# Optimization experiments

Measured on AMD Instinct MI355X. Metric: run time of the kernel, lower is better.

## Reference

```python
import jax, jax.numpy as jnp
import numpy as np

WINSIZE = 11
SIGMA = 1.5
L_RANGE = 1.0

def _gaussian_window(winsize, channel, dtype=jnp.float32):
    x = jnp.arange(winsize, dtype=dtype)
    g = jnp.exp(-((x - winsize // 2) ** 2) / (2.0 * SIGMA ** 2))
    g = g / g.sum()
    w2d = jnp.outer(g, g)                      # [ws, ws]
    # depthwise kernel [channel, 1, ws, ws] (OIHW, feature_group_count=channel)
    return jnp.broadcast_to(w2d, (channel, 1, winsize, winsize))

def _dwconv(x, w, channel):
    pad = WINSIZE // 2
    return jax.lax.conv_general_dilated(
        x, w, window_strides=(1, 1), padding=[(pad, pad), (pad, pad)],
        dimension_numbers=('NCHW', 'OIHW', 'NCHW'),
        feature_group_count=channel)

def _ssim(X, Y):
    channel = X.shape[1]
    w = _gaussian_window(WINSIZE, channel, X.dtype)
    mu1 = _dwconv(X, w, channel)
    mu2 = _dwconv(Y, w, channel)
    mu1_sq = mu1 * mu1
    mu2_sq = mu2 * mu2
    mu1_mu2 = mu1 * mu2
    sigma1_sq = _dwconv(X * X, w, channel) - mu1_sq
    sigma2_sq = _dwconv(Y * Y, w, channel) - mu2_sq
    sigma12 = _dwconv(X * Y, w, channel) - mu1_mu2
    C1 = (0.01 * L_RANGE) ** 2
    C2 = (0.03 * L_RANGE) ** 2
    ssim_map = ((2.0 * mu1_mu2 + C1) * (2.0 * sigma12 + C2)) / \
               ((mu1_sq + mu2_sq + C1) * (sigma1_sq + sigma2_sq + C2))
    return jnp.mean(ssim_map)  # sizeavg=True

def setup_inputs() -> dict:
    key = jax.random.key(0)
    k1, k2 = jax.random.split(key)
    shape = (16, 3, 512, 512)
    X = jax.random.uniform(k1, shape, dtype=jnp.float32)
    Y = jax.random.uniform(k2, shape, dtype=jnp.float32)
    return {"X": X, "Y": Y}

def reference(X, Y):
    return 1.0 - _ssim(X, Y)
```

## Files before the change

kernel.cpp:

```cpp
#include <hip/hip_runtime.h>


#define ROWS 32
#define COLS 256
#define NI   (ROWS + 10)
#define LW   (COLS + 10)
#define NIMG 48
#define NBLOCKS (NIMG * 2 * 16)
#define NPIXEL 12582912.0

__global__ __launch_bounds__(256) void ssim_row_kernel(
    const float* __restrict__ X, const float* __restrict__ Y,
    float* __restrict__ partial)
{
    __shared__ float sb[2][2][LW + 6];

    const int tid = threadIdx.x;
    const int bid = blockIdx.x;
    const int img = bid >> 5;
    const int rem = bid & 31;
    const int c0  = (rem & 1) * COLS;
    const int r0  = (rem >> 1) * ROWS;

    const float* __restrict__ Xi = X + (size_t)img * (512 * 512);
    const float* __restrict__ Yi = Y + (size_t)img * (512 * 512);

    float g[11];
    {
        float s = 0.f;
        #pragma unroll
        for (int i = 0; i < 11; ++i) {
            float d = (float)(i - 5);
            float e = expf(-d * d * (1.0f / 4.5f));
            g[i] = e; s += e;
        }
        float inv = 1.0f / s;
        #pragma unroll
        for (int i = 0; i < 11; ++i) g[i] *= inv;
    }

    const bool tail = (tid < LW - COLS);
    const int  gc0  = c0 - 5 + tid;
    const int  gc1  = gc0 + COLS;

    {
        int gr = r0 - 5;
        float x0 = 0.f, y0 = 0.f, x1 = 0.f, y1 = 0.f;
        if ((unsigned)gr < 512u) {
            const float* xr = Xi + (size_t)gr * 512;
            const float* yr = Yi + (size_t)gr * 512;
            if ((unsigned)gc0 < 512u) { x0 = xr[gc0]; y0 = yr[gc0]; }
            if (tail && (unsigned)gc1 < 512u) { x1 = xr[gc1]; y1 = yr[gc1]; }
        }
        sb[0][0][tid] = x0; sb[0][1][tid] = y0;
        if (tail) { sb[0][0][tid + COLS] = x1; sb[0][1][tid + COLS] = y1; }
    }
    __syncthreads();

    float ring[5][11];
    float acc = 0.f;

    const float C1 = 1e-4f, C2 = 9e-4f;

    #pragma unroll 1
    for (int jb = 0; jb < 44; jb += 11) {
        #pragma unroll
        for (int ph = 0; ph < 11; ++ph) {
            int j = jb + ph;
            if (j < NI) {
                const int cur = j & 1, nxt = cur ^ 1;
                const int jn = j + 1;

                float nx0 = 0.f, ny0 = 0.f, nx1 = 0.f, ny1 = 0.f;
                if (jn < NI) {
                    int gr = r0 - 5 + jn;
                    if ((unsigned)gr < 512u) {
                        const float* xr = Xi + (size_t)gr * 512;
                        const float* yr = Yi + (size_t)gr * 512;
                        if ((unsigned)gc0 < 512u) { nx0 = xr[gc0]; ny0 = yr[gc0]; }
                        if (tail && (unsigned)gc1 < 512u) { nx1 = xr[gc1]; ny1 = yr[gc1]; }
                    }
                }

                {
                    float hx = 0.f, hy = 0.f, hxx = 0.f, hyy = 0.f, hxy = 0.f;
                    #pragma unroll
                    for (int k = 0; k < 11; ++k) {
                        float x = sb[cur][0][tid + k];
                        float y = sb[cur][1][tid + k];
                        float w = g[k];
                        float wx = w * x, wy = w * y;
                        hx += wx; hy += wy;
                        hxx = fmaf(wx, x, hxx);
                        hyy = fmaf(wy, y, hyy);
                        hxy = fmaf(wx, y, hxy);
                    }
                    ring[0][ph] = hx;  ring[1][ph] = hy;
                    ring[2][ph] = hxx; ring[3][ph] = hyy; ring[4][ph] = hxy;
                }

                if (j >= 10) {
                    float mu1 = 0.f, mu2 = 0.f, vxx = 0.f, vyy = 0.f, vxy = 0.f;
                    #pragma unroll
                    for (int k = 0; k < 11; ++k) {
                        const int s = (ph + 1 + k) % 11;
                        float w = g[k];
                        mu1 = fmaf(w, ring[0][s], mu1);
                        mu2 = fmaf(w, ring[1][s], mu2);
                        vxx = fmaf(w, ring[2][s], vxx);
                        vyy = fmaf(w, ring[3][s], vyy);
                        vxy = fmaf(w, ring[4][s], vxy);
                    }
                    float m11 = mu1 * mu1, m22 = mu2 * mu2, m12 = mu1 * mu2;
                    float s1 = vxx - m11, s2 = vyy - m22, s12 = vxy - m12;
                    float num = (2.f * m12 + C1) * (2.f * s12 + C2);
                    float den = (m11 + m22 + C1) * (s1 + s2 + C2);
                    acc = fmaf(num, __builtin_amdgcn_rcpf(den), acc);
                }

                if (jn < NI) {
                    sb[nxt][0][tid] = nx0; sb[nxt][1][tid] = ny0;
                    if (tail) { sb[nxt][0][tid + COLS] = nx1; sb[nxt][1][tid + COLS] = ny1; }
                }
                __syncthreads();
            }
        }
    }

    #pragma unroll
    for (int off = 32; off > 0; off >>= 1)
        acc += __shfl_down(acc, off, 64);

    __shared__ float wsum[4];
    const int lane = tid & 63, wid = tid >> 6;
    if (lane == 0) wsum[wid] = acc;
    __syncthreads();
    if (tid == 0)
        partial[bid] = wsum[0] + wsum[1] + wsum[2] + wsum[3];
}

__global__ __launch_bounds__(256) void ssim_reduce_kernel(
    const float* __restrict__ partial, float* __restrict__ out)
{
    const int tid = threadIdx.x;
    double s = 0.0;
    for (int i = tid; i < NBLOCKS; i += 256) s += (double)partial[i];
    __shared__ double sd[256];
    sd[tid] = s;
    __syncthreads();
    for (int off = 128; off > 0; off >>= 1) {
        if (tid < off) sd[tid] += sd[tid + off];
        __syncthreads();
    }
    if (tid == 0) out[0] = (float)(1.0 - sd[0] / NPIXEL);
}

extern "C" void kernel_launch(void* const* d_in, const int* in_sizes, int n_in,
                              void* d_out, int out_size, void* d_ws, size_t ws_size,
                              hipStream_t stream) {
    const float* X = (const float*)d_in[0];
    const float* Y = (const float*)d_in[1];
    float* partial = (float*)d_ws;
    float* out = (float*)d_out;

    ssim_row_kernel<<<NBLOCKS, 256, 0, stream>>>(X, Y, partial);
    ssim_reduce_kernel<<<1, 256, 0, stream>>>(partial, out);
}
```

Measured before the change: 70.84 us.

## Rewrite SSIM as fp16 MFMA banded-matrix separable convolution

Replaces the scalar row-streaming separable Gaussian with a tile kernel that loads a padded 48x152 fp16 tile into shared memory. Both the horizontal and vertical 11-tap passes run as banded-matrix multiplies on MFMA units. Intermediate horizontal results are stored as fp16 in LDS. This is meant to move the convolution FLOPs from VALU to matrix cores and remove the per-row syncthreads. In exchange it adds fp16 rounding of the inputs, their squares and the intermediates, which can hurt accuracy in the variance terms (E[x^2]-mu^2 cancellation). It also uses more blocks, with halo overhead from 128-wide tiles.

```diff
diff --git a/kernel.cpp b/kernel.cpp
--- a/kernel.cpp
+++ b/kernel.cpp
@@ -1,26 +1,34 @@
 #include <hip/hip_runtime.h>
-
-
-#define ROWS 32
-#define COLS 256
-#define NI   (ROWS + 10)
-#define LW   (COLS + 10)
-#define NIMG 48
-#define NBLOCKS (NIMG * 2 * 16)
-#define NPIXEL 12582912.0
-
-__global__ __launch_bounds__(256) void ssim_row_kernel(
+#include <hip/hip_fp16.h>
+
+
+typedef _Float16 f16x8 __attribute__((ext_vector_type(8)));
+typedef _Float16 f16x4 __attribute__((ext_vector_type(4)));
+typedef float    f32x4 __attribute__((ext_vector_type(4)));
+
+#define BR 32
+#define BC 128
+#define SR 48
+#define SC 152
+#define HR 56
+#define NBLK (48 * 16 * 4)
+#define NPIX 12582912.0
+
+__global__ __launch_bounds__(256) void ssim_mfma_kernel(
     const float* __restrict__ X, const float* __restrict__ Y,
     float* __restrict__ partial)
 {
-    __shared__ float sb[2][2][LW + 6];
+    __shared__ __align__(16) _Float16 sbX[SR][SC];
+    __shared__ __align__(16) _Float16 sbY[SR][SC];
+    __shared__ __align__(16) _Float16 Hb[4][5][16][HR];
 
     const int tid = threadIdx.x;
     const int bid = blockIdx.x;
-    const int img = bid >> 5;
-    const int rem = bid & 31;
-    const int c0  = (rem & 1) * COLS;
-    const int r0  = (rem >> 1) * ROWS;
+    const int img = bid >> 6;
+    const int rb  = (bid >> 2) & 15;
+    const int cb  = bid & 3;
+    const int r0  = rb * BR;
+    const int c0  = cb * BC;
 
     const float* __restrict__ Xi = X + (size_t)img * (512 * 512);
     const float* __restrict__ Yi = Y + (size_t)img * (512 * 512);
@@ -39,92 +47,117 @@
         for (int i = 0; i < 11; ++i) g[i] *= inv;
     }
 
-    const bool tail = (tid < LW - COLS);
-    const int  gc0  = c0 - 5 + tid;
-    const int  gc1  = gc0 + COLS;
-
-    {
-        int gr = r0 - 5;
-        float x0 = 0.f, y0 = 0.f, x1 = 0.f, y1 = 0.f;
-        if ((unsigned)gr < 512u) {
-            const float* xr = Xi + (size_t)gr * 512;
-            const float* yr = Yi + (size_t)gr * 512;
-            if ((unsigned)gc0 < 512u) { x0 = xr[gc0]; y0 = yr[gc0]; }
-            if (tail && (unsigned)gc1 < 512u) { x1 = xr[gc1]; y1 = yr[gc1]; }
-        }
-        sb[0][0][tid] = x0; sb[0][1][tid] = y0;
-        if (tail) { sb[0][0][tid + COLS] = x1; sb[0][1][tid + COLS] = y1; }
+    const int lane = tid & 63;
+    const int jj   = lane & 15;
+    const int gq   = lane >> 4;
+
+    f16x8 wfrag;
+    #pragma unroll
+    for (int v = 0; v < 8; ++v) {
+        int k = 8 * gq + v, d = k - jj;
+        wfrag[v] = (_Float16)((d >= 0 && d <= 10) ? g[d] : 0.f);
+    }
+    f16x8 gv32[2];
+    f16x4 gv16[2];
+    #pragma unroll
+    for (int rt = 0; rt < 2; ++rt) {
+        int r = 16 * rt + jj;
+        #pragma unroll
+        for (int v = 0; v < 8; ++v) {
+            int k = 8 * gq + v, d = k - r;
+            gv32[rt][v] = (_Float16)((d >= 0 && d <= 10) ? g[d] : 0.f);
+        }
+        #pragma unroll
+        for (int v = 0; v < 4; ++v) {
+            int k = 32 + 4 * gq + v, d = k - r;
+            gv16[rt][v] = (_Float16)((d >= 0 && d <= 10) ? g[d] : 0.f);
+        }
+    }
+
+    for (int idx = tid; idx < SR * SC; idx += 256) {
+        int row = idx / SC;
+        int q   = idx - row * SC;
+        int gr = r0 - 5 + row, gc = c0 - 5 + q;
+        float xv = 0.f, yv = 0.f;
+        if ((unsigned)gr < 512u && (unsigned)gc < 512u) {
+            size_t o = (size_t)gr * 512 + (size_t)gc;
+            xv = Xi[o]; yv = Yi[o];
+        }
+        sbX[row][q] = (_Float16)xv;
+        sbY[row][q] = (_Float16)yv;
     }
     __syncthreads();
 
-    float ring[5][11];
+    const int w = tid >> 6;
     float acc = 0.f;
 
-    const float C1 = 1e-4f, C2 = 9e-4f;
-
     #pragma unroll 1
-    for (int jb = 0; jb < 44; jb += 11) {
-        #pragma unroll
-        for (int ph = 0; ph < 11; ++ph) {
-            int j = jb + ph;
-            if (j < NI) {
-                const int cur = j & 1, nxt = cur ^ 1;
-                const int jn = j + 1;
-
-                float nx0 = 0.f, ny0 = 0.f, nx1 = 0.f, ny1 = 0.f;
-                if (jn < NI) {
-                    int gr = r0 - 5 + jn;
-                    if ((unsigned)gr < 512u) {
-                        const float* xr = Xi + (size_t)gr * 512;
-                        const float* yr = Yi + (size_t)gr * 512;
-                        if ((unsigned)gc0 < 512u) { nx0 = xr[gc0]; ny0 = yr[gc0]; }
-                        if (tail && (unsigned)gc1 < 512u) { nx1 = xr[gc1]; ny1 = yr[gc1]; }
-                    }
-                }
-
-                {
-                    float hx = 0.f, hy = 0.f, hxx = 0.f, hyy = 0.f, hxy = 0.f;
-                    #pragma unroll
-                    for (int k = 0; k < 11; ++k) {
-                        float x = sb[cur][0][tid + k];
-                        float y = sb[cur][1][tid + k];
-                        float w = g[k];
-                        float wx = w * x, wy = w * y;
-                        hx += wx; hy += wy;
-                        hxx = fmaf(wx, x, hxx);
-                        hyy = fmaf(wy, y, hyy);
-                        hxy = fmaf(wx, y, hxy);
-                    }
-                    ring[0][ph] = hx;  ring[1][ph] = hy;
-                    ring[2][ph] = hxx; ring[3][ph] = hyy; ring[4][ph] = hxy;
-                }
-
-                if (j >= 10) {
-                    float mu1 = 0.f, mu2 = 0.f, vxx = 0.f, vyy = 0.f, vxy = 0.f;
-                    #pragma unroll
-                    for (int k = 0; k < 11; ++k) {
-                        const int s = (ph + 1 + k) % 11;
-                        float w = g[k];
-                        mu1 = fmaf(w, ring[0][s], mu1);
-                        mu2 = fmaf(w, ring[1][s], mu2);
-                        vxx = fmaf(w, ring[2][s], vxx);
-                        vyy = fmaf(w, ring[3][s], vyy);
-                        vxy = fmaf(w, ring[4][s], vxy);
-                    }
-                    float m11 = mu1 * mu1, m22 = mu2 * mu2, m12 = mu1 * mu2;
-                    float s1 = vxx - m11, s2 = vyy - m22, s12 = vxy - m12;
-                    float num = (2.f * m12 + C1) * (2.f * s12 + C2);
-                    float den = (m11 + m22 + C1) * (s1 + s2 + C2);
-                    acc = fmaf(num, __builtin_amdgcn_rcpf(den), acc);
-                }
-
-                if (jn < NI) {
-                    sb[nxt][0][tid] = nx0; sb[nxt][1][tid] = ny0;
-                    if (tail) { sb[nxt][0][tid + COLS] = nx1; sb[nxt][1][tid + COLS] = ny1; }
-                }
-                __syncthreads();
+    for (int t = 0; t < 2; ++t) {
+        const int jt = 2 * w + t;
+
+        f32x4 hacc[3][5];
+        #pragma unroll
+        for (int rt = 0; rt < 3; ++rt)
+            #pragma unroll
+            for (int m = 0; m < 5; ++m) hacc[rt][m] = (f32x4)0.f;
+
+        #pragma unroll
+        for (int rt = 0; rt < 3; ++rt) {
+            const f16x8 ax = *(const f16x8*)&sbX[16 * rt + jj][16 * jt + 8 * gq];
+            const f16x8 ay = *(const f16x8*)&sbY[16 * rt + jj][16 * jt + 8 * gq];
+            const f16x8 axx = ax * ax;
+            const f16x8 ayy = ay * ay;
+            const f16x8 axy = ax * ay;
+            hacc[rt][0] = __builtin_amdgcn_mfma_f32_16x16x32_f16(ax,  wfrag, hacc[rt][0], 0, 0, 0);
+            hacc[rt][1] = __builtin_amdgcn_mfma_f32_16x16x32_f16(ay,  wfrag, hacc[rt][1], 0, 0, 0);
+            hacc[rt][2] = __builtin_amdgcn_mfma_f32_16x16x32_f16(axx, wfrag, hacc[rt][2], 0, 0, 0);
+            hacc[rt][3] = __builtin_amdgcn_mfma_f32_16x16x32_f16(ayy, wfrag, hacc[rt][3], 0, 0, 0);
+            hacc[rt][4] = __builtin_amdgcn_mfma_f32_16x16x32_f16(axy, wfrag, hacc[rt][4], 0, 0, 0);
+        }
+
+        #pragma unroll
+        for (int rt = 0; rt < 3; ++rt)
+            #pragma unroll
+            for (int m = 0; m < 5; ++m) {
+                const int rbase = 16 * rt + 4 * gq;
+                f32x4 c = hacc[rt][m];
+                _Float16* p = &Hb[w][m][jj][rbase];
+                p[0] = (_Float16)c[0];
+                p[1] = (_Float16)c[1];
+                p[2] = (_Float16)c[2];
+                p[3] = (_Float16)c[3];
             }
-        }
+        asm volatile("s_waitcnt lgkmcnt(0)" ::: "memory");
+
+        f32x4 vacc[2][5];
+        #pragma unroll
+        for (int rt = 0; rt < 2; ++rt)
+            #pragma unroll
+            for (int m = 0; m < 5; ++m) vacc[rt][m] = (f32x4)0.f;
+
+        #pragma unroll
+        for (int m = 0; m < 5; ++m) {
+            const f16x8 b0 = *(const f16x8*)&Hb[w][m][jj][8 * gq];
+            const f16x4 b1 = *(const f16x4*)&Hb[w][m][jj][32 + 4 * gq];
+            vacc[0][m] = __builtin_amdgcn_mfma_f32_16x16x32_f16(gv32[0], b0, vacc[0][m], 0, 0, 0);
+            vacc[1][m] = __builtin_amdgcn_mfma_f32_16x16x32_f16(gv32[1], b0, vacc[1][m], 0, 0, 0);
+            vacc[0][m] = __builtin_amdgcn_mfma_f32_16x16x16f16(gv16[0], b1, vacc[0][m], 0, 0, 0);
+            vacc[1][m] = __builtin_amdgcn_mfma_f32_16x16x16f16(gv16[1], b1, vacc[1][m], 0, 0, 0);
+        }
+
+        const float C1 = 1e-4f, C2 = 9e-4f;
+        #pragma unroll
+        for (int rt = 0; rt < 2; ++rt)
+            #pragma unroll
+            for (int e = 0; e < 4; ++e) {
+                float mu1 = vacc[rt][0][e], mu2 = vacc[rt][1][e];
+                float exx = vacc[rt][2][e], eyy = vacc[rt][3][e], exy = vacc[rt][4][e];
+                float m11 = mu1 * mu1, m22 = mu2 * mu2, m12 = mu1 * mu2;
+                float s1 = exx - m11, s2 = eyy - m22, s12 = exy - m12;
+                float num = (2.f * m12 + C1) * (2.f * s12 + C2);
+                float den = (m11 + m22 + C1) * (s1 + s2 + C2);
+                acc = fmaf(num, __builtin_amdgcn_rcpf(den), acc);
+            }
     }
 
     #pragma unroll
@@ -132,8 +165,7 @@
         acc += __shfl_down(acc, off, 64);
 
     __shared__ float wsum[4];
-    const int lane = tid & 63, wid = tid >> 6;
-    if (lane == 0) wsum[wid] = acc;
+    if (lane == 0) wsum[w] = acc;
     __syncthreads();
     if (tid == 0)
         partial[bid] = wsum[0] + wsum[1] + wsum[2] + wsum[3];
@@ -144,7 +176,7 @@
 {
     const int tid = threadIdx.x;
     double s = 0.0;
-    for (int i = tid; i < NBLOCKS; i += 256) s += (double)partial[i];
+    for (int i = tid; i < NBLK; i += 256) s += (double)partial[i];
     __shared__ double sd[256];
     sd[tid] = s;
     __syncthreads();
@@ -152,7 +184,7 @@
         if (tid < off) sd[tid] += sd[tid + off];
         __syncthreads();
     }
-    if (tid == 0) out[0] = (float)(1.0 - sd[0] / NPIXEL);
+    if (tid == 0) out[0] = (float)(1.0 - sd[0] / NPIX);
 }
 
 extern "C" void kernel_launch(void* const* d_in, const int* in_sizes, int n_in,
@@ -163,6 +195,6 @@
     float* partial = (float*)d_ws;
     float* out = (float*)d_out;
 
-    ssim_row_kernel<<<NBLOCKS, 256, 0, stream>>>(X, Y, partial);
+    ssim_mfma_kernel<<<NBLK, 256, 0, stream>>>(X, Y, partial);
     ssim_reduce_kernel<<<1, 256, 0, stream>>>(partial, out);
 }
```

Result: slower. 107.2 us (+51.3%).
